# Kernel optimization log

Hardware: AMD Instinct MI355X
Metric: run time of the kernel (lower is better)

## Reference

```python
import jax, jax.numpy as jnp
import numpy as np

K = 16
D = 1024
B = 65536

# Row-major off-diagonal index order matching the torch double loop (i, j, i != j)
_ii, _jj = np.nonzero(~np.eye(K, dtype=bool))  # each (K*(K-1),), row-major
OFF_I = jnp.asarray(_ii)
OFF_J = jnp.asarray(_jj)
DIAG = jnp.arange(K)


def setup_inputs() -> dict:
    key = jax.random.key(0)
    k1, k2, k3, k4, k5 = jax.random.split(key, 5)
    scale_d = 1.0 / np.sqrt(D)
    return {
        "x": jax.random.normal(k1, (B, D), dtype=jnp.float32),
        "Wd": jax.random.normal(k2, (K, D), dtype=jnp.float32) * scale_d,
        "bd": jax.random.normal(k3, (K,), dtype=jnp.float32) * 0.1,
        "Wo": jax.random.normal(k4, (K * (K - 1), D), dtype=jnp.float32) * scale_d,
        "bo": jax.random.normal(k5, (K * (K - 1),), dtype=jnp.float32) * 0.1 - 3.0,
    }


def reference(x, Wd, bd, Wo, bo):
    # Diagonal gates: (B, K)
    c_diag = jax.nn.sigmoid(jnp.einsum("bd,kd->bk", x, Wd) + bd)
    # Off-diagonal values: (B, K*(K-1)), non-positive
    off_vals = -jax.nn.softplus(jnp.einsum("bd,kd->bk", x, Wo) + bo)
    C = jnp.zeros((x.shape[0], K, K), dtype=x.dtype)
    C = C.at[:, OFF_I, OFF_J].set(off_vals)
    C = C.at[:, DIAG, DIAG].set(c_diag)
    return C
```

## Files before the change

### kernel.cpp

```cpp
#include <hip/hip_runtime.h>
#include <hip/hip_bf16.h>
#include <stdint.h>


typedef __bf16 bf16x8 __attribute__((ext_vector_type(8)));
typedef float f32x4 __attribute__((ext_vector_type(4)));

#define THREADS 256
#define BM 64
#define KSTEPS 32
#define WIMG 16384
#define WBYTES (WIMG * KSTEPS)

#define ASLOT 8192
#define BBASE 24576
#define BSLOT 16384
#define SMEM_SZ 73728

__device__ __forceinline__ unsigned bf_rtne(unsigned u) {
  return (u + 0x7fffu + ((u >> 16) & 1u)) >> 16;
}
__device__ __forceinline__ unsigned pack2(float lo, float hi) {
  return bf_rtne(__float_as_uint(lo)) | (bf_rtne(__float_as_uint(hi)) << 16);
}
__device__ __forceinline__ bf16x8 packfrag(const f32x4& a, const f32x4& b) {
  uint4 u;
  u.x = pack2(a[0], a[1]); u.y = pack2(a[2], a[3]);
  u.z = pack2(b[0], b[1]); u.w = pack2(b[2], b[3]);
  return *reinterpret_cast<bf16x8*>(&u);
}
__device__ __forceinline__ void gload_lds16(const void* g, void* l) {
  __builtin_amdgcn_global_load_lds(
      (const __attribute__((address_space(1))) unsigned int*)g,
      (__attribute__((address_space(3))) unsigned int*)l, 16, 0, 0);
}

__global__ void prep_kernel(const float* __restrict__ Wd, const float* __restrict__ bd,
                            const float* __restrict__ Wo, const float* __restrict__ bo,
                            char* __restrict__ wbuf, float* __restrict__ bias) {
  const int c = blockIdx.x;
  const int t = threadIdx.x;
  const int i = c >> 4, j = c & 15;
  const float* src;
  float b;
  if (i == j) { src = Wd + i * 1024; b = bd[i]; }
  else { int r = i * 15 + (j < i ? j : j - 1); src = Wo + r * 1024; b = bo[r]; }
  if (t == 0) bias[c] = b;
  const int kk = t * 4;
  const int img = kk >> 5, k5 = kk & 31;
  float4 v = *reinterpret_cast<const float4*>(src + kk);
  uint2 h;
  h.x = pack2(v.x, v.y);
  h.y = pack2(v.z, v.w);
  const unsigned off = (unsigned)((c * 64 + k5 * 2) ^ (((c >> 1) & 3) << 4));
  *reinterpret_cast<uint2*>(wbuf + img * WIMG + off) = h;
}

__global__ __launch_bounds__(THREADS, 2) void cap_main(
    const float* __restrict__ x, const char* __restrict__ wbuf,
    const float* __restrict__ bias, float* __restrict__ out) {
  __shared__ char smem[SMEM_SZ];

  const int tid = threadIdx.x;
  const int wid = tid >> 6;
  const int lane = tid & 63;
  const int l15 = lane & 15;
  const int l4 = lane >> 4;
  const int l7 = lane & 7;
  const int l3 = lane >> 3;

  const size_t blkRow = (size_t)blockIdx.x * BM;

  const float* asrc0 = x + (blkRow + (size_t)((wid * 2 + 0) * 8 + l3)) * 1024 + ((l7 * 4) ^ (l3 << 2));
  const float* asrc1 = x + (blkRow + (size_t)((wid * 2 + 1) * 8 + l3)) * 1024 + ((l7 * 4) ^ (l3 << 2));
  const unsigned adst0 = (unsigned)((wid * 2 + 0) * 1024 + lane * 16);
  const unsigned adst1 = (unsigned)((wid * 2 + 1) * 1024 + lane * 16);

  const unsigned swA = (unsigned)((l15 & 7) << 4);
  const unsigned swB = (unsigned)(((l15 >> 1) & 3) << 4);
  const unsigned bbase = (unsigned)(((wid * 64 + l15) * 64 + l4 * 16) ^ swB);

  f32x4 acc[4][4];
#pragma unroll
  for (int m = 0; m < 4; ++m)
#pragma unroll
    for (int n = 0; n < 4; ++n) acc[m][n] = (f32x4){0.f, 0.f, 0.f, 0.f};

#define STAGE(CH, ASL, BSL)                                                     \
  {                                                                             \
    gload_lds16(asrc0 + (CH) * 32, smem + (ASL) + adst0);                       \
    gload_lds16(asrc1 + (CH) * 32, smem + (ASL) + adst1);                       \
    const char* wsp = wbuf + (CH) * WIMG;                                       \
    _Pragma("unroll") for (int i = 0; i < 4; ++i)                               \
        gload_lds16(wsp + (wid * 4 + i) * 1024 + lane * 16,                     \
                    smem + (BSL) + (wid * 4 + i) * 1024 + lane * 16);           \
  }

  STAGE(0, 0, BBASE);
  STAGE(1, ASLOT, BBASE + BSLOT);
  asm volatile("s_waitcnt vmcnt(6)\n\ts_barrier" ::: "memory");

  unsigned aR = 0, bR = BBASE;
  unsigned aI = 2 * ASLOT, bI = BBASE + 2 * BSLOT;

  for (int t = 0; t < KSTEPS; ++t) {
    const int ch = (t + 2 < KSTEPS) ? t + 2 : KSTEPS - 1;
    STAGE(ch, aI, bI);

    const char* Ac = smem + aR;
    const char* Bc = smem + bR;
    bf16x8 af[4], bfr[4];
#pragma unroll
    for (int m = 0; m < 4; ++m) {
      const unsigned rb = (unsigned)((m * 16 + l15) * 128);
      f32x4 u0 = *reinterpret_cast<const f32x4*>(Ac + rb + ((l4 * 32) ^ swA));
      f32x4 u1 = *reinterpret_cast<const f32x4*>(Ac + rb + ((l4 * 32 + 16) ^ swA));
      af[m] = packfrag(u0, u1);
    }
#pragma unroll
    for (int n = 0; n < 4; ++n)
      bfr[n] = *reinterpret_cast<const bf16x8*>(Bc + bbase + n * 1024);

#pragma unroll
    for (int m = 0; m < 4; ++m)
#pragma unroll
      for (int n = 0; n < 4; ++n)
        acc[m][n] = __builtin_amdgcn_mfma_f32_16x16x32_bf16(af[m], bfr[n], acc[m][n], 0, 0, 0);

    asm volatile("s_waitcnt vmcnt(6)\n\ts_barrier" ::: "memory");

    aR = (aR == 2 * ASLOT) ? 0u : aR + ASLOT;
    aI = (aI == 2 * ASLOT) ? 0u : aI + ASLOT;
    bR = (bR == BBASE + 2 * BSLOT) ? (unsigned)BBASE : bR + BSLOT;
    bI = (bI == BBASE + 2 * BSLOT) ? (unsigned)BBASE : bI + BSLOT;
  }
#undef STAGE

  asm volatile("s_waitcnt vmcnt(0)" ::: "memory");
  __syncthreads();

  float bs[4];
#pragma unroll
  for (int n = 0; n < 4; ++n) bs[n] = bias[wid * 64 + n * 16 + l15];

  const int rr2 = tid >> 4;
  const int co = (tid & 15) * 16;
  const char* rdp = smem + rr2 * 1040 + co * 4;

#pragma unroll
  for (int p = 0; p < 4; ++p) {
#pragma unroll
    for (int n = 0; n < 4; ++n) {
      const int col = wid * 64 + n * 16 + l15;
      const bool diag = (col % 17) == 0;
#pragma unroll
      for (int j2 = 0; j2 < 4; ++j2) {
        const int rr = l4 * 4 + j2;
        float v = acc[p][n][j2] + bs[n];
        float e = __expf(-fabsf(v));
        float sig = (v >= 0.f) ? 1.f / (1.f + e) : e / (1.f + e);
        float sp = fmaxf(v, 0.f) + __logf(1.f + e);
        *reinterpret_cast<float*>(smem + rr * 1040 + col * 4) = diag ? sig : -sp;
      }
    }
    __syncthreads();
    float4 o0 = *reinterpret_cast<const float4*>(rdp);
    float4 o1 = *reinterpret_cast<const float4*>(rdp + 16);
    float4 o2 = *reinterpret_cast<const float4*>(rdp + 32);
    float4 o3 = *reinterpret_cast<const float4*>(rdp + 48);
    float* orow = out + (blkRow + (size_t)(p * 16 + rr2)) * 256 + co;
    *reinterpret_cast<float4*>(orow) = o0;
    *reinterpret_cast<float4*>(orow + 4) = o1;
    *reinterpret_cast<float4*>(orow + 8) = o2;
    *reinterpret_cast<float4*>(orow + 12) = o3;
    __syncthreads();
  }
}

extern "C" void kernel_launch(void* const* d_in, const int* in_sizes, int n_in,
                              void* d_out, int out_size, void* d_ws, size_t ws_size,
                              hipStream_t stream) {
  const float* x = (const float*)d_in[0];
  const float* Wd = (const float*)d_in[1];
  const float* bd = (const float*)d_in[2];
  const float* Wo = (const float*)d_in[3];
  const float* bo = (const float*)d_in[4];
  float* out = (float*)d_out;
  char* wbuf = (char*)d_ws;
  float* bias = (float*)(wbuf + WBYTES);

  prep_kernel<<<dim3(256), dim3(256), 0, stream>>>(Wd, bd, Wo, bo, wbuf, bias);
  cap_main<<<dim3(1024), dim3(THREADS), 0, stream>>>(x, wbuf, bias, out);
}
```

Measured before the change: 106.6 us.

## Double row tile to 128 with 8 waves, sharing B tile across row halves

```diff
diff --git a/kernel.cpp b/kernel.cpp
--- a/kernel.cpp
+++ b/kernel.cpp
@@ -6,16 +6,16 @@
 typedef __bf16 bf16x8 __attribute__((ext_vector_type(8)));
 typedef float f32x4 __attribute__((ext_vector_type(4)));
 
-#define THREADS 256
-#define BM 64
+#define THREADS 512
+#define BM 128
 #define KSTEPS 32
 #define WIMG 16384
 #define WBYTES (WIMG * KSTEPS)
 
-#define ASLOT 8192
-#define BBASE 24576
+#define ASLOT 16384
+#define BBASE 49152
 #define BSLOT 16384
-#define SMEM_SZ 73728
+#define SMEM_SZ 81920
 
 __device__ __forceinline__ unsigned bf_rtne(unsigned u) {
   return (u + 0x7fffu + ((u >> 16) & 1u)) >> 16;
@@ -56,7 +56,7 @@
   *reinterpret_cast<uint2*>(wbuf + img * WIMG + off) = h;
 }
 
-__global__ __launch_bounds__(THREADS, 2) void cap_main(
+__global__ __launch_bounds__(THREADS, 4) void cap_main(
     const float* __restrict__ x, const char* __restrict__ wbuf,
     const float* __restrict__ bias, float* __restrict__ out) {
   __shared__ char smem[SMEM_SZ];
@@ -66,19 +66,24 @@
   const int lane = tid & 63;
   const int l15 = lane & 15;
   const int l4 = lane >> 4;
-  const int l7 = lane & 7;
-  const int l3 = lane >> 3;
+  const int wm = wid >> 2;
+  const int wn = wid & 3;
 
   const size_t blkRow = (size_t)blockIdx.x * BM;
 
-  const float* asrc0 = x + (blkRow + (size_t)((wid * 2 + 0) * 8 + l3)) * 1024 + ((l7 * 4) ^ (l3 << 2));
-  const float* asrc1 = x + (blkRow + (size_t)((wid * 2 + 1) * 8 + l3)) * 1024 + ((l7 * 4) ^ (l3 << 2));
-  const unsigned adst0 = (unsigned)((wid * 2 + 0) * 1024 + lane * 16);
-  const unsigned adst1 = (unsigned)((wid * 2 + 1) * 1024 + lane * 16);
+  const unsigned acol = (unsigned)(((tid & 7) * 16) ^ (((tid >> 3) & 7) << 4));
+  const char* asrc[2];
+  unsigned adst[2];
+#pragma unroll
+  for (int i = 0; i < 2; ++i) {
+    const int row = i * 64 + (tid >> 3);
+    asrc[i] = (const char*)(x + (blkRow + (size_t)row) * 1024) + acol;
+    adst[i] = (unsigned)(i * 8192 + tid * 16);
+  }
 
   const unsigned swA = (unsigned)((l15 & 7) << 4);
-  const unsigned swB = (unsigned)(((l15 >> 1) & 3) << 4);
-  const unsigned bbase = (unsigned)(((wid * 64 + l15) * 64 + l4 * 16) ^ swB);
+  const unsigned bbase = (unsigned)(wn * 4096 + l15 * 64 +
+                                    ((l4 * 16) ^ (((l15 >> 1) & 3) << 4)));
 
   f32x4 acc[4][4];
 #pragma unroll
@@ -86,33 +91,40 @@
 #pragma unroll
     for (int n = 0; n < 4; ++n) acc[m][n] = (f32x4){0.f, 0.f, 0.f, 0.f};
 
-#define STAGE(CH, ASL, BSL)                                                     \
-  {                                                                             \
-    gload_lds16(asrc0 + (CH) * 32, smem + (ASL) + adst0);                       \
-    gload_lds16(asrc1 + (CH) * 32, smem + (ASL) + adst1);                       \
-    const char* wsp = wbuf + (CH) * WIMG;                                       \
-    _Pragma("unroll") for (int i = 0; i < 4; ++i)                               \
-        gload_lds16(wsp + (wid * 4 + i) * 1024 + lane * 16,                     \
-                    smem + (BSL) + (wid * 4 + i) * 1024 + lane * 16);           \
-  }
-
-  STAGE(0, 0, BBASE);
-  STAGE(1, ASLOT, BBASE + BSLOT);
-  asm volatile("s_waitcnt vmcnt(6)\n\ts_barrier" ::: "memory");
-
-  unsigned aR = 0, bR = BBASE;
-  unsigned aI = 2 * ASLOT, bI = BBASE + 2 * BSLOT;
+#define STAGE_A(CH, SL)                                                        \
+  {                                                                            \
+    _Pragma("unroll") for (int i = 0; i < 2; ++i)                              \
+        gload_lds16(asrc[i] + (CH) * 128, smem + (SL) + adst[i]);              \
+  }
+#define STAGE_B(CH, SL)                                                        \
+  {                                                                            \
+    const char* wsp = wbuf + (CH) * WIMG;                                      \
+    _Pragma("unroll") for (int i = 0; i < 2; ++i)                              \
+        gload_lds16(wsp + i * 8192 + tid * 16,                                 \
+                    smem + BBASE + (SL) + i * 8192 + tid * 16);                \
+  }
+
+  STAGE_A(0, 0);
+  STAGE_B(0, 0);
+  STAGE_A(1, ASLOT);
+  asm volatile("s_waitcnt vmcnt(2)\n\ts_barrier" ::: "memory");
+
+  unsigned aR = 0;
+  unsigned aI = 2 * ASLOT;
+  unsigned bR = 0;
 
   for (int t = 0; t < KSTEPS; ++t) {
-    const int ch = (t + 2 < KSTEPS) ? t + 2 : KSTEPS - 1;
-    STAGE(ch, aI, bI);
+    const int tb = (t + 1 < KSTEPS) ? t + 1 : KSTEPS - 1;
+    STAGE_B(tb, bR ^ BSLOT);
+    const int ta = (t + 2 < KSTEPS) ? t + 2 : KSTEPS - 1;
+    STAGE_A(ta, aI);
 
     const char* Ac = smem + aR;
-    const char* Bc = smem + bR;
+    const char* Bc = smem + BBASE + bR;
     bf16x8 af[4], bfr[4];
 #pragma unroll
     for (int m = 0; m < 4; ++m) {
-      const unsigned rb = (unsigned)((m * 16 + l15) * 128);
+      const unsigned rb = (unsigned)((wm * 64 + m * 16 + l15) * 128);
       f32x4 u0 = *reinterpret_cast<const f32x4*>(Ac + rb + ((l4 * 32) ^ swA));
       f32x4 u1 = *reinterpret_cast<const f32x4*>(Ac + rb + ((l4 * 32 + 16) ^ swA));
       af[m] = packfrag(u0, u1);
@@ -127,52 +139,53 @@
       for (int n = 0; n < 4; ++n)
         acc[m][n] = __builtin_amdgcn_mfma_f32_16x16x32_bf16(af[m], bfr[n], acc[m][n], 0, 0, 0);
 
-    asm volatile("s_waitcnt vmcnt(6)\n\ts_barrier" ::: "memory");
+    asm volatile("s_waitcnt vmcnt(2)" ::: "memory");
+    asm volatile("s_waitcnt lgkmcnt(0)" ::: "memory");
+    __builtin_amdgcn_s_barrier();
 
     aR = (aR == 2 * ASLOT) ? 0u : aR + ASLOT;
     aI = (aI == 2 * ASLOT) ? 0u : aI + ASLOT;
-    bR = (bR == BBASE + 2 * BSLOT) ? (unsigned)BBASE : bR + BSLOT;
-    bI = (bI == BBASE + 2 * BSLOT) ? (unsigned)BBASE : bI + BSLOT;
-  }
-#undef STAGE
+    bR ^= BSLOT;
+  }
+#undef STAGE_A
+#undef STAGE_B
 
   asm volatile("s_waitcnt vmcnt(0)" ::: "memory");
   __syncthreads();
 
   float bs[4];
 #pragma unroll
-  for (int n = 0; n < 4; ++n) bs[n] = bias[wid * 64 + n * 16 + l15];
-
-  const int rr2 = tid >> 4;
-  const int co = (tid & 15) * 16;
+  for (int n = 0; n < 4; ++n) bs[n] = bias[wn * 64 + n * 16 + l15];
+
+  const int rr2 = tid >> 5;
+  const int co = (tid & 31) * 8;
   const char* rdp = smem + rr2 * 1040 + co * 4;
 
 #pragma unroll
-  for (int p = 0; p < 4; ++p) {
-#pragma unroll
-    for (int n = 0; n < 4; ++n) {
-      const int col = wid * 64 + n * 16 + l15;
-      const bool diag = (col % 17) == 0;
-#pragma unroll
-      for (int j2 = 0; j2 < 4; ++j2) {
-        const int rr = l4 * 4 + j2;
-        float v = acc[p][n][j2] + bs[n];
-        float e = __expf(-fabsf(v));
-        float sig = (v >= 0.f) ? 1.f / (1.f + e) : e / (1.f + e);
-        float sp = fmaxf(v, 0.f) + __logf(1.f + e);
-        *reinterpret_cast<float*>(smem + rr * 1040 + col * 4) = diag ? sig : -sp;
+  for (int p = 0; p < 8; ++p) {
+    if ((wid >> 2) == (p >> 2)) {
+      const int m = p & 3;
+#pragma unroll
+      for (int n = 0; n < 4; ++n) {
+        const int col = wn * 64 + n * 16 + l15;
+        const bool diag = (col % 17) == 0;
+#pragma unroll
+        for (int j2 = 0; j2 < 4; ++j2) {
+          const int rr = l4 * 4 + j2;
+          float v = acc[m][n][j2] + bs[n];
+          float e = __expf(-fabsf(v));
+          float sig = (v >= 0.f) ? 1.f / (1.f + e) : e / (1.f + e);
+          float sp = fmaxf(v, 0.f) + __logf(1.f + e);
+          *reinterpret_cast<float*>(smem + rr * 1040 + col * 4) = diag ? sig : -sp;
+        }
       }
     }
     __syncthreads();
     float4 o0 = *reinterpret_cast<const float4*>(rdp);
     float4 o1 = *reinterpret_cast<const float4*>(rdp + 16);
-    float4 o2 = *reinterpret_cast<const float4*>(rdp + 32);
-    float4 o3 = *reinterpret_cast<const float4*>(rdp + 48);
     float* orow = out + (blkRow + (size_t)(p * 16 + rr2)) * 256 + co;
     *reinterpret_cast<float4*>(orow) = o0;
     *reinterpret_cast<float4*>(orow + 4) = o1;
-    *reinterpret_cast<float4*>(orow + 8) = o2;
-    *reinterpret_cast<float4*>(orow + 12) = o3;
     __syncthreads();
   }
 }
@@ -190,5 +203,5 @@
   float* bias = (float*)(wbuf + WBYTES);
 
   prep_kernel<<<dim3(256), dim3(256), 0, stream>>>(Wd, bd, Wo, bo, wbuf, bias);
-  cap_main<<<dim3(1024), dim3(THREADS), 0, stream>>>(x, wbuf, bias, out);
-}
+  cap_main<<<dim3(512), dim3(THREADS), 0, stream>>>(x, wbuf, bias, out);
+}
```

Measured after the change: 103.0 us. -3.4%, faster.
